# Optimization experiments

Hardware: AMD Instinct MI355X
Metric: run time of the kernel (lower is better)

The kernel has to match this reference:

```python
import jax, jax.numpy as jnp
import numpy as np

H_OUT = 8
W_OUT = 8
MAXG = 4  # max adaptive sampling grid per bin: ceil((H-1)/H_OUT) with H=32


def _flip_table():
    h, w = H_OUT, W_OUT
    ys = np.repeat(np.arange(h), w)
    xs = np.tile(np.arange(w), h)
    rys = np.repeat(np.arange(h - 1, -1, -1), w)
    # NOTE: original torch code does arange(w-1,-1,-1).reshape(h,1).repeat(1,w)
    # which makes reverse_xs a per-ROW reversal (requires h==w); replicated faithfully.
    rxs = np.repeat(np.arange(w - 1, -1, -1), w)
    i00 = ys * w + xs
    i01 = ys * w + rxs
    i10 = rys * w + xs
    i11 = rys * w + rxs
    # original stacks [i00, i01, i01, i10, i11]; idx_idxs in {0..3} so entry for
    # (y_rev=1,x_rev=0) is i01 (duplicated) and (1,1) hits i10; i11 is unused. Replicated.
    return jnp.asarray(np.stack([i00, i01, i01, i10, i11]), dtype=jnp.int32)

_TABLE = _flip_table()


def _axis_samples(start, bin_sz, grid, n_out, size):
    # start, bin_sz: [N] float; grid: [N] int (adaptive samples per bin along this axis)
    # returns low/high neighbor indices and corner weights, each [N, n_out*MAXG]
    N = start.shape[0]
    g_safe = jnp.maximum(grid, 1).astype(start.dtype)
    ph = jnp.arange(n_out, dtype=start.dtype)
    i = jnp.arange(MAXG, dtype=start.dtype)
    pos = (start[:, None, None]
           + ph[None, :, None] * bin_sz[:, None, None]
           + (i[None, None, :] + 0.5) * (bin_sz / g_safe)[:, None, None])  # [N,n_out,MAXG]
    valid = ((pos >= -1.0) & (pos <= size)
             & (jnp.arange(MAXG)[None, None, :] < grid[:, None, None]))
    p = jnp.clip(pos, 0.0, size - 1)
    low = jnp.floor(p).astype(jnp.int32)
    high = jnp.minimum(low + 1, size - 1)
    l = p - low.astype(p.dtype)
    vf = valid.astype(start.dtype)
    return (low.reshape(N, -1), high.reshape(N, -1),
            ((1.0 - l) * vf).reshape(N, -1), (l * vf).reshape(N, -1))


def _roi_align_flip(feats, batch_idxs, starts, goals):
    B, C, H, W = feats.shape
    N = starts.shape[0]
    s = starts.astype(feats.dtype)
    g = goals.astype(feats.dtype)
    y_min = jnp.minimum(s[:, 0], g[:, 0]); y_max = jnp.maximum(s[:, 0], g[:, 0])
    x_min = jnp.minimum(s[:, 1], g[:, 1]); x_max = jnp.maximum(s[:, 1], g[:, 1])
    y_rev = s[:, 0] > g[:, 0]
    x_rev = s[:, 1] > g[:, 1]
    # torchvision roi_align: aligned=True, spatial_scale=1.0, sampling_ratio=-1
    start_h = y_min - 0.5; start_w = x_min - 0.5
    roi_h = y_max - y_min; roi_w = x_max - x_min
    bin_h = roi_h / H_OUT; bin_w = roi_w / W_OUT
    gh = jnp.ceil(bin_h).astype(jnp.int32)
    gw = jnp.ceil(bin_w).astype(jnp.int32)
    count = jnp.maximum(gh * gw, 1).astype(feats.dtype)
    ylo, yhi, wy0, wy1 = _axis_samples(start_h, bin_h, gh, H_OUT, H)  # [N, H_OUT*MAXG]
    xlo, xhi, wx0, wx1 = _axis_samples(start_w, bin_w, gw, W_OUT, W)  # [N, W_OUT*MAXG]
    fv = feats.reshape(B, C, H * W)[batch_idxs]  # [N,C,H*W] per-box feature slab
    hM, wM = H_OUT * MAXG, W_OUT * MAXG

    def gath(yi, xi):
        lin = (yi[:, :, None] * W + xi[:, None, :]).reshape(N, 1, hM * wM)
        v = jnp.take_along_axis(fv, jnp.broadcast_to(lin, (N, C, hM * wM)), axis=2)
        return v.reshape(N, C, hM, wM)

    def outer(a, b):
        return a[:, None, :, None] * b[:, None, None, :]

    acc = (gath(ylo, xlo) * outer(wy0, wx0)
           + gath(ylo, xhi) * outer(wy0, wx1)
           + gath(yhi, xlo) * outer(wy1, wx0)
           + gath(yhi, xhi) * outer(wy1, wx1))  # [N,C,hM,wM]
    rois = acc.reshape(N, C, H_OUT, MAXG, W_OUT, MAXG).sum(axis=(3, 5))
    rois = rois / count[:, None, None, None]
    # per-box orientation flip via index-table gather
    idx_idxs = y_rev.astype(jnp.int32) * 2 + x_rev.astype(jnp.int32)
    sel = _TABLE[idx_idxs]  # [N, h*w]
    rflat = rois.reshape(N, C, H_OUT * W_OUT)
    out = jnp.take_along_axis(rflat, jnp.broadcast_to(sel[:, None, :], rflat.shape), axis=2)
    return out.reshape(N, C, H_OUT, W_OUT)


def setup_inputs() -> dict:
    key = jax.random.key(0)
    k1, k2, k3, k4 = jax.random.split(key, 4)
    B, C, H, W = 8, 64, 32, 32
    N = 1024  # B * A with A = 128 agents
    feats = jax.random.normal(k1, (B, C, H, W), dtype=jnp.float32)
    batch_idxs = jax.random.randint(k2, (N,), 0, B, dtype=jnp.int32)
    starts = jax.random.randint(k3, (N, 2), 0, H, dtype=jnp.int32)
    goals = jax.random.randint(k4, (N, 2), 0, H, dtype=jnp.int32)
    return {"feats": feats, "batch_idxs": batch_idxs, "starts": starts, "goals": goals}


def reference(feats, batch_idxs, starts, goals):
    return _roi_align_flip(feats, batch_idxs, starts, goals)
```

## Files before the change

### kernel.cpp

```cpp
#include <hip/hip_runtime.h>

#define H_OUT 8
#define W_OUT 8
#define MAXG 4
#define CCHUNK 8

__global__ __launch_bounds__(256) void ordered_roi_kernel(
    const float* __restrict__ feats,
    const int*   __restrict__ batch_idxs,
    const int*   __restrict__ starts,
    const int*   __restrict__ goals,
    float*       __restrict__ out,
    int C, int CG)
{
    const int bx  = blockIdx.x;
    const int n   = bx / CG;
    const int cg  = bx - n * CG;
    const int tid = threadIdx.x;

    const float s0 = (float)starts[2 * n + 0];
    const float s1 = (float)starts[2 * n + 1];
    const float g0 = (float)goals[2 * n + 0];
    const float g1 = (float)goals[2 * n + 1];
    const float y_min = fminf(s0, g0), y_max = fmaxf(s0, g0);
    const float x_min = fminf(s1, g1), x_max = fmaxf(s1, g1);
    const bool  y_rev = s0 > g0;
    const bool  x_rev = s1 > g1;
    const float start_h = y_min - 0.5f;
    const float start_w = x_min - 0.5f;
    const float bin_h = (y_max - y_min) / (float)H_OUT;
    const float bin_w = (x_max - x_min) / (float)W_OUT;
    const int   gh = (int)ceilf(bin_h);
    const int   gw = (int)ceilf(bin_w);
    const float inv_count = 1.0f / fmaxf((float)(gh * gw), 1.0f);

    __shared__ int   s_lo[2][H_OUT * MAXG];
    __shared__ int   s_hi[2][H_OUT * MAXG];
    __shared__ float s_w0[2][H_OUT * MAXG];
    __shared__ float s_w1[2][H_OUT * MAXG];
    __shared__ float s_t[CCHUNK][H_OUT][33];

    if (tid < 64) {
        const int axis = tid >> 5;
        const int k    = tid & 31;
        const int ph   = k >> 2;
        const int i    = k & 3;
        const float start = axis ? start_w : start_h;
        const float bin   = axis ? bin_w  : bin_h;
        const int   grid  = axis ? gw     : gh;
        const float size  = 32.0f;
        const float gsafe = (float)(grid > 1 ? grid : 1);
        const float pos = start + (float)ph * bin + ((float)i + 0.5f) * (bin / gsafe);
        const bool  valid = (pos >= -1.0f) && (pos <= size) && (i < grid);
        const float p  = fminf(fmaxf(pos, 0.0f), size - 1.0f);
        const int   lo = (int)floorf(p);
        const int   hi = min(lo + 1, 31);
        const float l  = p - (float)lo;
        const float vf = valid ? 1.0f : 0.0f;
        s_lo[axis][k] = lo;
        s_hi[axis][k] = hi;
        s_w0[axis][k] = (1.0f - l) * vf;
        s_w1[axis][k] = l * vf;
    }
    __syncthreads();

    const int py_a = (tid >> 5) & 7;
    const int x_a  = tid & 31;

    int   yloR[MAXG], yhiR[MAXG];
    float wy0R[MAXG], wy1R[MAXG];
    #pragma unroll
    for (int iy = 0; iy < MAXG; ++iy) {
        const int ky = py_a * MAXG + iy;
        yloR[iy] = s_lo[0][ky] * 32 + x_a;
        yhiR[iy] = s_hi[0][ky] * 32 + x_a;
        wy0R[iy] = s_w0[0][ky];
        wy1R[iy] = s_w1[0][ky];
    }

    const int b = batch_idxs[n];
    const float* __restrict__ fb = feats + ((size_t)b * C + (size_t)cg * CCHUNK) * 1024;

    #pragma unroll
    for (int c = 0; c < CCHUNK; ++c) {
        const float* __restrict__ fc = fb + c * 1024;
        float acc = 0.0f;
        #pragma unroll
        for (int iy = 0; iy < MAXG; ++iy) {
            if (iy < gh) {
                acc += wy0R[iy] * fc[yloR[iy]] + wy1R[iy] * fc[yhiR[iy]];
            }
        }
        s_t[c][py_a][x_a] = acc;
    }
    __syncthreads();

    const int yx = tid & 63;
    const int y  = yx >> 3;
    const int xo = yx & 7;
    const int c0 = tid >> 6;

    int py, px;
    if (y_rev && x_rev)      { py = H_OUT - 1 - y; px = xo; }
    else if (y_rev || x_rev) { py = y;             px = W_OUT - 1 - y; }
    else                     { py = y;             px = xo; }

    float acc0 = 0.0f, acc1 = 0.0f;
    #pragma unroll
    for (int ix = 0; ix < MAXG; ++ix) {
        if (ix < gw) {
            const int   kx  = px * MAXG + ix;
            const int   xlo = s_lo[1][kx];
            const int   xhi = s_hi[1][kx];
            const float wx0 = s_w0[1][kx];
            const float wx1 = s_w1[1][kx];
            acc0 += wx0 * s_t[c0][py][xlo]     + wx1 * s_t[c0][py][xhi];
            acc1 += wx0 * s_t[c0 + 4][py][xlo] + wx1 * s_t[c0 + 4][py][xhi];
        }
    }

    float* __restrict__ ob = out + ((size_t)n * C + (size_t)cg * CCHUNK) * (H_OUT * W_OUT);
    ob[tid]       = acc0 * inv_count;
    ob[tid + 256] = acc1 * inv_count;
}

extern "C" void kernel_launch(void* const* d_in, const int* in_sizes, int n_in,
                              void* d_out, int out_size, void* d_ws, size_t ws_size,
                              hipStream_t stream) {
    const float* feats      = (const float*)d_in[0];
    const int*   batch_idxs = (const int*)d_in[1];
    const int*   starts     = (const int*)d_in[2];
    const int*   goals      = (const int*)d_in[3];
    float*       out        = (float*)d_out;

    const int N  = in_sizes[1];
    const int C  = out_size / (N * H_OUT * W_OUT);
    const int CG = C / CCHUNK;

    ordered_roi_kernel<<<N * CG, 256, 0, stream>>>(feats, batch_idxs, starts, goals,
                                                   out, C, CG);
}
```

Measured before the change: 82.75 us.

## Merge bilinear sample taps into per-bin contiguous row weights with float4 loads

Rather than storing lo/hi index and weight pairs for each sample, each output bin's samples are collapsed into a contiguous range of source rows or columns with accumulated weights (up to six slots). The row pass then reads each needed row once as float4 vectors covering four columns and two channels per thread, and the column pass reads each column once. This removes duplicate loads of shared neighbor rows and cuts instruction count. The trade-off is data-dependent loop bounds replacing fully unrolled loops.

```diff
diff --git a/kernel.cpp b/kernel.cpp
--- a/kernel.cpp
+++ b/kernel.cpp
@@ -4,6 +4,7 @@
 #define W_OUT 8
 #define MAXG 4
 #define CCHUNK 8
+#define RSLOTS 6
 
 __global__ __launch_bounds__(256) void ordered_roi_kernel(
     const float* __restrict__ feats,
@@ -34,64 +35,68 @@
     const int   gw = (int)ceilf(bin_w);
     const float inv_count = 1.0f / fmaxf((float)(gh * gw), 1.0f);
 
-    __shared__ int   s_lo[2][H_OUT * MAXG];
-    __shared__ int   s_hi[2][H_OUT * MAXG];
-    __shared__ float s_w0[2][H_OUT * MAXG];
-    __shared__ float s_w1[2][H_OUT * MAXG];
+    __shared__ int   s_rbase[2][H_OUT];
+    __shared__ int   s_rcnt[2][H_OUT];
+    __shared__ float s_rw[2][H_OUT][RSLOTS];
     __shared__ float s_t[CCHUNK][H_OUT][33];
 
-    if (tid < 64) {
-        const int axis = tid >> 5;
-        const int k    = tid & 31;
-        const int ph   = k >> 2;
-        const int i    = k & 3;
+    if (tid < 16) {
+        const int axis = tid >> 3;
+        const int ph   = tid & 7;
         const float start = axis ? start_w : start_h;
         const float bin   = axis ? bin_w  : bin_h;
         const int   grid  = axis ? gw     : gh;
-        const float size  = 32.0f;
         const float gsafe = (float)(grid > 1 ? grid : 1);
-        const float pos = start + (float)ph * bin + ((float)i + 0.5f) * (bin / gsafe);
-        const bool  valid = (pos >= -1.0f) && (pos <= size) && (i < grid);
-        const float p  = fminf(fmaxf(pos, 0.0f), size - 1.0f);
-        const int   lo = (int)floorf(p);
-        const int   hi = min(lo + 1, 31);
-        const float l  = p - (float)lo;
-        const float vf = valid ? 1.0f : 0.0f;
-        s_lo[axis][k] = lo;
-        s_hi[axis][k] = hi;
-        s_w0[axis][k] = (1.0f - l) * vf;
-        s_w1[axis][k] = l * vf;
+        float wloc[RSLOTS] = {0.f, 0.f, 0.f, 0.f, 0.f, 0.f};
+        int base = 0, last = -1;
+        for (int i = 0; i < grid && i < MAXG; ++i) {
+            const float pos = start + (float)ph * bin + ((float)i + 0.5f) * (bin / gsafe);
+            const float vf  = (pos >= -1.0f && pos <= 32.0f) ? 1.0f : 0.0f;
+            const float p   = fminf(fmaxf(pos, 0.0f), 31.0f);
+            const int   lo  = (int)floorf(p);
+            const int   hi  = min(lo + 1, 31);
+            const float l   = p - (float)lo;
+            if (i == 0) base = lo;
+            wloc[lo - base] += (1.0f - l) * vf;
+            wloc[hi - base] += l * vf;
+            last = hi;
+        }
+        s_rbase[axis][ph] = base;
+        s_rcnt[axis][ph]  = (grid > 0) ? (last - base + 1) : 0;
+        #pragma unroll
+        for (int k = 0; k < RSLOTS; ++k) s_rw[axis][ph][k] = wloc[k];
     }
     __syncthreads();
 
-    const int py_a = (tid >> 5) & 7;
-    const int x_a  = tid & 31;
+    {
+        const int cp = tid >> 6;
+        const int py = (tid >> 3) & 7;
+        const int xq = tid & 7;
+        const int rb = s_rbase[0][py];
+        const int rc = s_rcnt[0][py];
 
-    int   yloR[MAXG], yhiR[MAXG];
-    float wy0R[MAXG], wy1R[MAXG];
-    #pragma unroll
-    for (int iy = 0; iy < MAXG; ++iy) {
-        const int ky = py_a * MAXG + iy;
-        yloR[iy] = s_lo[0][ky] * 32 + x_a;
-        yhiR[iy] = s_hi[0][ky] * 32 + x_a;
-        wy0R[iy] = s_w0[0][ky];
-        wy1R[iy] = s_w1[0][ky];
-    }
+        const int b = batch_idxs[n];
+        const float* __restrict__ fb =
+            feats + ((size_t)b * C + (size_t)cg * CCHUNK) * 1024;
+        const float* __restrict__ fc0 = fb + (size_t)cp * 1024 + xq * 4;
+        const float* __restrict__ fc1 = fc0 + 4 * 1024;
 
-    const int b = batch_idxs[n];
-    const float* __restrict__ fb = feats + ((size_t)b * C + (size_t)cg * CCHUNK) * 1024;
-
-    #pragma unroll
-    for (int c = 0; c < CCHUNK; ++c) {
-        const float* __restrict__ fc = fb + c * 1024;
-        float acc = 0.0f;
-        #pragma unroll
-        for (int iy = 0; iy < MAXG; ++iy) {
-            if (iy < gh) {
-                acc += wy0R[iy] * fc[yloR[iy]] + wy1R[iy] * fc[yhiR[iy]];
-            }
+        float a00 = 0.f, a01 = 0.f, a02 = 0.f, a03 = 0.f;
+        float a10 = 0.f, a11 = 0.f, a12 = 0.f, a13 = 0.f;
+        for (int j = 0; j < rc; ++j) {
+            const float w = s_rw[0][py][j];
+            const float4 r0 = *reinterpret_cast<const float4*>(fc0 + (rb + j) * 32);
+            const float4 r1 = *reinterpret_cast<const float4*>(fc1 + (rb + j) * 32);
+            a00 = fmaf(w, r0.x, a00); a01 = fmaf(w, r0.y, a01);
+            a02 = fmaf(w, r0.z, a02); a03 = fmaf(w, r0.w, a03);
+            a10 = fmaf(w, r1.x, a10); a11 = fmaf(w, r1.y, a11);
+            a12 = fmaf(w, r1.z, a12); a13 = fmaf(w, r1.w, a13);
         }
-        s_t[c][py_a][x_a] = acc;
+        const int x0 = xq * 4;
+        s_t[cp][py][x0 + 0] = a00; s_t[cp][py][x0 + 1] = a01;
+        s_t[cp][py][x0 + 2] = a02; s_t[cp][py][x0 + 3] = a03;
+        s_t[cp + 4][py][x0 + 0] = a10; s_t[cp + 4][py][x0 + 1] = a11;
+        s_t[cp + 4][py][x0 + 2] = a12; s_t[cp + 4][py][x0 + 3] = a13;
     }
     __syncthreads();
 
@@ -105,21 +110,17 @@
     else if (y_rev || x_rev) { py = y;             px = W_OUT - 1 - y; }
     else                     { py = y;             px = xo; }
 
+    const int xb = s_rbase[1][px];
+    const int xc = s_rcnt[1][px];
     float acc0 = 0.0f, acc1 = 0.0f;
-    #pragma unroll
-    for (int ix = 0; ix < MAXG; ++ix) {
-        if (ix < gw) {
-            const int   kx  = px * MAXG + ix;
-            const int   xlo = s_lo[1][kx];
-            const int   xhi = s_hi[1][kx];
-            const float wx0 = s_w0[1][kx];
-            const float wx1 = s_w1[1][kx];
-            acc0 += wx0 * s_t[c0][py][xlo]     + wx1 * s_t[c0][py][xhi];
-            acc1 += wx0 * s_t[c0 + 4][py][xlo] + wx1 * s_t[c0 + 4][py][xhi];
-        }
+    for (int j = 0; j < xc; ++j) {
+        const float w = s_rw[1][px][j];
+        acc0 = fmaf(w, s_t[c0][py][xb + j],     acc0);
+        acc1 = fmaf(w, s_t[c0 + 4][py][xb + j], acc1);
     }
 
-    float* __restrict__ ob = out + ((size_t)n * C + (size_t)cg * CCHUNK) * (H_OUT * W_OUT);
+    float* __restrict__ ob =
+        out + ((size_t)n * C + (size_t)cg * CCHUNK) * (H_OUT * W_OUT);
     ob[tid]       = acc0 * inv_count;
     ob[tid + 256] = acc1 * inv_count;
 }
```

Result: no change. 83.71 us (+1.2%).
